# Optimization experiments

Hardware: AMD Instinct MI355X
Metric: run time of the kernel (lower is better)

The kernel has to match this reference:

```python
import jax, jax.numpy as jnp
import numpy as np

N_NODES, N_EDGES = 50000, 800000
IN_DIM, OUT_DIM, EDGE_DIM = 128, 128, 32
NUM_HEADS = 8
HEAD_DIM = OUT_DIM // NUM_HEADS
SCALE = HEAD_DIM ** -0.5


def setup_inputs() -> dict:
    key = jax.random.key(0)
    ks = jax.random.split(key, 8)
    def lin_w(k, fan_in, fan_out):
        # kaiming-uniform-ish init like nn.Linear
        bound = 1.0 / np.sqrt(fan_in)
        return jax.random.uniform(k, (fan_in, fan_out), jnp.float32, -bound, bound)
    return {
        "node_features": jax.random.normal(ks[0], (N_NODES, IN_DIM), jnp.float32),
        "edge_features": jax.random.normal(ks[1], (N_EDGES, EDGE_DIM), jnp.float32),
        "Wq": lin_w(ks[2], IN_DIM, OUT_DIM), "bq": jnp.zeros((OUT_DIM,), jnp.float32),
        "Wk": lin_w(ks[3], IN_DIM, OUT_DIM), "bk": jnp.zeros((OUT_DIM,), jnp.float32),
        "Wv": lin_w(ks[4], IN_DIM, OUT_DIM), "bv": jnp.zeros((OUT_DIM,), jnp.float32),
        "We": lin_w(ks[5], EDGE_DIM, OUT_DIM), "be": jnp.zeros((OUT_DIM,), jnp.float32),
        "edge_list": jax.random.randint(ks[6], (N_EDGES, 2), 0, N_NODES, jnp.int32),
        "num_nodes": N_NODES,
    }


def reference(node_features, edge_features, Wq, bq, Wk, bk, Wv, bv, We, be, edge_list, num_nodes):
    # node projections -> [N, H, D]
    Q = (node_features @ Wq + bq).reshape(-1, NUM_HEADS, HEAD_DIM)
    K = (node_features @ Wk + bk).reshape(-1, NUM_HEADS, HEAD_DIM)
    V = (node_features @ Wv + bv).reshape(-1, NUM_HEADS, HEAD_DIM)
    edge_bias = (edge_features @ We + be).reshape(-1, NUM_HEADS, HEAD_DIM)

    src = edge_list[:, 0]  # node_in
    dst = edge_list[:, 1]  # node_out

    # per-edge per-head scores: [E, H]
    scores = jnp.einsum("ehd,ehd->eh", Q[src], K[dst]) * SCALE + edge_bias.sum(-1)
    # NOTE: softmax over the HEADS axis (dim=1), exactly as in the source
    weights = jax.nn.softmax(scores, axis=1)

    # weighted messages gathered from src, scattered to dst: [E, H, D] -> [N, H, D]
    msg = V[src] * weights[..., None]
    node_updates = jax.ops.segment_sum(msg, dst, num_segments=num_nodes)
    return node_updates.reshape(num_nodes, OUT_DIM)
```

## Files before the change

kernel.cpp:

```cpp
#include <hip/hip_runtime.h>
#include <math.h>

#define IN_DIM   128
#define OUT_DIM  128
#define EDGE_DIM 32
#define NUM_HEADS 8
#define HEAD_DIM 16
#define SCALE 0.25f
#define CSTRIDE 16
#define MAXDEG 48

typedef __attribute__((ext_vector_type(8))) short bf16x8;
typedef __attribute__((ext_vector_type(4))) float f32x4;
typedef __attribute__((ext_vector_type(2))) float f32x2;
typedef __attribute__((ext_vector_type(4))) unsigned int u32x4;

__device__ inline unsigned short f2bf(float x) {
    unsigned int u = __float_as_uint(x);
    unsigned int r = u + 0x7fff + ((u >> 16) & 1);
    return (unsigned short)(r >> 16);
}
__device__ inline float bflo(unsigned int u) { return __uint_as_float(u << 16); }
__device__ inline float bfhi(unsigned int u) { return __uint_as_float(u & 0xffff0000u); }
__device__ inline f32x2 up2(unsigned int u) {
    f32x2 r; r[0] = bflo(u); r[1] = bfhi(u); return r;
}

__global__ __launch_bounds__(256) void setup_kernel(
    int* __restrict__ counts, int n_nodes, int nbz,
    const float* __restrict__ Wq, const float* __restrict__ Wk,
    const float* __restrict__ Wv, unsigned short* __restrict__ WtB, int nbw,
    const float* __restrict__ We, const float* __restrict__ be,
    float* __restrict__ WeR, float* __restrict__ beR,
    const float* __restrict__ X, unsigned short* __restrict__ Xb)
{
    const int bx = blockIdx.x;
    const int t  = threadIdx.x;
    if (bx < nbz) {
        const int i = bx * 256 + t;
        if (i < n_nodes) counts[i << 4] = 0;
    } else if (bx < nbz + nbw) {
        const int idx = (bx - nbz) * 256 + t;
        const int mat = idx >> 14;
        const int rem = idx & 16383;
        const int n = rem >> 7, k = rem & 127;
        const float* W = (mat == 0) ? Wq : (mat == 1) ? Wk : Wv;
        WtB[mat * 16384 + n * 128 + k] = f2bf(W[k * 128 + n]);
    } else if (bx == nbz + nbw) {
        const int k = t >> 3, h = t & 7;
        float s = 0.f;
#pragma unroll
        for (int d = 0; d < HEAD_DIM; ++d) s += We[k * OUT_DIM + h * HEAD_DIM + d];
        WeR[k * NUM_HEADS + h] = s;
        if (t < NUM_HEADS) {
            float sb = 0.f;
#pragma unroll
            for (int d = 0; d < HEAD_DIM; ++d) sb += be[t * HEAD_DIM + d];
            beR[t] = sb;
        }
    } else {
        const int i = (bx - (nbz + nbw + 1)) * 256 + t;
        if (i < n_nodes * 16) {
            const f32x4* xr = (const f32x4*)(X + (size_t)i * 8);
            const f32x4 x0 = xr[0], x1 = xr[1];
            u32x4 p;
            p[0] = (unsigned)f2bf(x0[0]) | ((unsigned)f2bf(x0[1]) << 16);
            p[1] = (unsigned)f2bf(x0[2]) | ((unsigned)f2bf(x0[3]) << 16);
            p[2] = (unsigned)f2bf(x1[0]) | ((unsigned)f2bf(x1[1]) << 16);
            p[3] = (unsigned)f2bf(x1[2]) | ((unsigned)f2bf(x1[3]) << 16);
            *(u32x4*)(Xb + (size_t)i * 8) = p;
        }
    }
}

__global__ __launch_bounds__(256) void qkv_kernel(
    const unsigned short* __restrict__ Xb, const unsigned short* __restrict__ WtB,
    const float* __restrict__ bq, const float* __restrict__ bk,
    const float* __restrict__ bv,
    unsigned short* __restrict__ QVb, unsigned short* __restrict__ Kb,
    int n_nodes, int nbm)
{
    __shared__ unsigned short shW[16384];
    const int bx = blockIdx.x;
    const int t  = threadIdx.x;

    const int which = bx / nbm;
    const int mb    = bx - which * nbm;
    const unsigned short* Wg = WtB + which * 16384;

#pragma unroll
    for (int kk = 0; kk < 8; ++kk) {
        const int c = kk * 256 + t;
        const u32x4 v = ((const u32x4*)Wg)[c];
        const int row = c >> 4;
        const int bir = (c & 15) << 4;
        *(u32x4*)((char*)shW + row * 256 + (bir ^ ((row & 7) << 4))) = v;
    }
    __syncthreads();

    const int wave = t >> 6, lane = t & 63;
    const int quad = lane >> 4, li = lane & 15;
    const int mbase = mb * 256 + wave * 64;

    int mrow[4];
#pragma unroll
    for (int m = 0; m < 4; ++m) {
        const int r_ = mbase + m * 16 + li;
        mrow[m] = (r_ < n_nodes) ? r_ : (n_nodes - 1);
    }

    f32x4 acc[4][8];
#pragma unroll
    for (int m = 0; m < 4; ++m)
#pragma unroll
        for (int nt = 0; nt < 8; ++nt) acc[m][nt] = (f32x4){0.f, 0.f, 0.f, 0.f};

#pragma unroll
    for (int ks = 0; ks < 4; ++ks) {
        bf16x8 a[4];
#pragma unroll
        for (int m = 0; m < 4; ++m)
            a[m] = *(const bf16x8*)(Xb + (size_t)mrow[m] * 128 + ks * 32 + quad * 8);
#pragma unroll
        for (int nt = 0; nt < 8; ++nt) {
            const int row = nt * 16 + li;
            const bf16x8 b = *(const bf16x8*)((const char*)shW + row * 256 +
                                ((ks * 64 + quad * 16) ^ ((row & 7) << 4)));
#pragma unroll
            for (int m = 0; m < 4; ++m)
                acc[m][nt] = __builtin_amdgcn_mfma_f32_16x16x32_bf16(a[m], b, acc[m][nt], 0, 0, 0);
        }
    }

    const float* bias = (which == 0) ? bq : (which == 1) ? bk : bv;
    float bv8[8];
#pragma unroll
    for (int nt = 0; nt < 8; ++nt) bv8[nt] = bias[nt * 16 + li];

    __syncthreads();

    unsigned short* stg = shW + wave * 2176;
    const int R = lane >> 2, cc4 = lane & 3;
#pragma unroll
    for (int m = 0; m < 4; ++m) {
#pragma unroll
        for (int nt = 0; nt < 8; ++nt)
#pragma unroll
            for (int r = 0; r < 4; ++r)
                stg[(quad * 4 + r) * 136 + nt * 16 + li] = f2bf(acc[m][nt][r] + bv8[nt]);
        __syncthreads();

        const int node = mbase + m * 16 + R;
        if (node < n_nodes) {
            const u32x4* s = (const u32x4*)(stg + R * 136 + cc4 * 32);
            u32x4 d0 = s[0], d1 = s[1], d2 = s[2], d3 = s[3];
            unsigned short* dp =
                (which == 0) ? (QVb + (size_t)node * 256 + cc4 * 32)
              : (which == 1) ? (Kb  + (size_t)node * 128 + cc4 * 32)
              :                (QVb + (size_t)node * 256 + 128 + cc4 * 32);
            u32x4* d = (u32x4*)dp;
            d[0] = d0; d[1] = d1; d[2] = d2; d[3] = d3;
        }
        __syncthreads();
    }
}

__global__ __launch_bounds__(256) void edge_kernel(
    const int* __restrict__ el, int* __restrict__ counts,
    const float* __restrict__ ef, const float* __restrict__ WeR,
    const float* __restrict__ beR, unsigned int* __restrict__ recs,
    int n_edges)
{
    const int e = blockIdx.x * 256 + threadIdx.x;
    if (e >= n_edges) return;
    const int2 ed = ((const int2*)el)[e];
    const int r = atomicAdd(&counts[ed.y << 4], 1);

    float acc[NUM_HEADS];
#pragma unroll
    for (int h = 0; h < NUM_HEADS; ++h) acc[h] = beR[h];

    const f32x4* efr = (const f32x4*)(ef + (size_t)e * EDGE_DIM);
#pragma unroll
    for (int kk = 0; kk < 8; ++kk) {
        const f32x4 f = efr[kk];
#pragma unroll
        for (int c = 0; c < 4; ++c) {
            const float* wr = WeR + (kk * 4 + c) * NUM_HEADS;
#pragma unroll
            for (int h = 0; h < NUM_HEADS; ++h)
                acc[h] = fmaf(f[c], wr[h], acc[h]);
        }
    }

    if (r < MAXDEG) {
        u32x4 r0, r1;
        r0[0] = (unsigned)ed.x;
        r0[1] = 0;
        r0[2] = (unsigned)f2bf(acc[0]) | ((unsigned)f2bf(acc[1]) << 16);
        r0[3] = (unsigned)f2bf(acc[2]) | ((unsigned)f2bf(acc[3]) << 16);
        r1[0] = (unsigned)f2bf(acc[4]) | ((unsigned)f2bf(acc[5]) << 16);
        r1[1] = (unsigned)f2bf(acc[6]) | ((unsigned)f2bf(acc[7]) << 16);
        r1[2] = 0; r1[3] = 0;
        u32x4* rp = (u32x4*)(recs + (size_t)(ed.y * MAXDEG + r) * 8);
        rp[0] = r0;
        rp[1] = r1;
    }
}

__global__ __launch_bounds__(256) void aggregate_kernel(
    const unsigned short* __restrict__ QVb, const unsigned short* __restrict__ Kb,
    const int* __restrict__ counts, const unsigned int* __restrict__ recs,
    float* __restrict__ out, int n_nodes, int nwtot)
{
    const int lane = threadIdx.x & 63;
    const int g = lane >> 3;
    const int h = lane & 7;
    const int ebd = 2 + (h >> 1);

    int node = (blockIdx.x * 256 + threadIdx.x) >> 6;
    if (node >= n_nodes) return;
    int cnt = counts[node << 4];
    if (cnt > MAXDEG) cnt = MAXDEG;

    for (;;) {
        const int nnode = node + nwtot;
        int ncnt = 0;
        if (nnode < n_nodes) {
            ncnt = counts[nnode << 4];
            if (ncnt > MAXDEG) ncnt = MAXDEG;
        }

        const int beg = node * MAXDEG;

        f32x2 kf[8];
        {
            const u32x4* kp = (const u32x4*)(Kb + (size_t)node * 128 + h * 16);
            const u32x4 ka = kp[0], kb_ = kp[1];
#pragma unroll
            for (int j = 0; j < 4; ++j) { kf[j] = up2(ka[j]); kf[4 + j] = up2(kb_[j]); }
        }

        f32x2 acc[8];
#pragma unroll
        for (int j = 0; j < 8; ++j) acc[j] = (f32x2){0.f, 0.f};

        if (cnt > 0) {
            const int last = cnt - 1;
            int s0 = g; if (s0 > last) s0 = last;
            const unsigned src_c = recs[(size_t)(beg + s0) * 8];
            unsigned ebw_c = recs[(size_t)(beg + s0) * 8 + ebd];
            const unsigned short* bp0 = QVb + (size_t)src_c * 256 + h * 16;
            u32x4 qa = *(const u32x4*)bp0;
            u32x4 qb = *(const u32x4*)(bp0 + 8);
            u32x4 va = *(const u32x4*)(bp0 + 128);
            u32x4 vb = *(const u32x4*)(bp0 + 136);
            int s1 = 8 + g; if (s1 > last) s1 = last;
            unsigned src_n = recs[(size_t)(beg + s1) * 8];
            unsigned ebw_n = recs[(size_t)(beg + s1) * 8 + ebd];

            for (int i = 0; i < cnt; i += 8) {
                int s2 = i + 16 + g; if (s2 > last) s2 = last;
                const unsigned src_f = recs[(size_t)(beg + s2) * 8];
                const unsigned ebw_f = recs[(size_t)(beg + s2) * 8 + ebd];
                const unsigned short* bp = QVb + (size_t)src_n * 256 + h * 16;
                const u32x4 qan = *(const u32x4*)bp;
                const u32x4 qbn = *(const u32x4*)(bp + 8);
                const u32x4 van = *(const u32x4*)(bp + 128);
                const u32x4 vbn = *(const u32x4*)(bp + 136);

                const float eb = (h & 1) ? bfhi(ebw_c) : bflo(ebw_c);
                f32x2 p2 = (f32x2){0.f, 0.f};
#pragma unroll
                for (int j = 0; j < 4; ++j) {
                    p2 += up2(qa[j]) * kf[j];
                    p2 += up2(qb[j]) * kf[4 + j];
                }
                const float score = fmaf(p2[0] + p2[1], SCALE, eb);

                const float ex = __expf(score);
                float den = ex;
                den += __shfl_xor(den, 1);
                den += __shfl_xor(den, 2);
                den += __shfl_xor(den, 4);
                float wgt = __fdividef(ex, den);
                if (i + g >= cnt) wgt = 0.f;
                const f32x2 w2 = (f32x2){wgt, wgt};
#pragma unroll
                for (int j = 0; j < 4; ++j) {
                    acc[j]     += up2(va[j]) * w2;
                    acc[4 + j] += up2(vb[j]) * w2;
                }

                qa = qan; qb = qbn; va = van; vb = vbn;
                ebw_c = ebw_n;
                src_n = src_f; ebw_n = ebw_f;
            }
        }

#pragma unroll
        for (int mask = 8; mask <= 32; mask <<= 1)
#pragma unroll
            for (int j = 0; j < 8; ++j) {
                f32x2 o;
                o[0] = __shfl_xor(acc[j][0], mask);
                o[1] = __shfl_xor(acc[j][1], mask);
                acc[j] += o;
            }

        float ox = 0.f, oy = 0.f;
#pragma unroll
        for (int j = 0; j < 8; ++j)
            if (g == j) { ox = acc[j][0]; oy = acc[j][1]; }
        *(float2*)(out + (size_t)node * OUT_DIM + h * 16 + g * 2) = make_float2(ox, oy);

        if (nnode >= n_nodes) break;
        node = nnode; cnt = ncnt;
    }
}

extern "C" void kernel_launch(void* const* d_in, const int* in_sizes, int n_in,
                              void* d_out, int out_size, void* d_ws, size_t ws_size,
                              hipStream_t stream)
{
    const float* X   = (const float*)d_in[0];
    const float* ef  = (const float*)d_in[1];
    const float* Wq  = (const float*)d_in[2];
    const float* bq  = (const float*)d_in[3];
    const float* Wk  = (const float*)d_in[4];
    const float* bk  = (const float*)d_in[5];
    const float* Wv  = (const float*)d_in[6];
    const float* bv  = (const float*)d_in[7];
    const float* We  = (const float*)d_in[8];
    const float* be  = (const float*)d_in[9];
    const int*   el  = (const int*)d_in[10];

    const int n_nodes = in_sizes[0] / IN_DIM;
    const int n_edges = in_sizes[10] / 2;

    char* w = (char*)d_ws;
    auto alloc = [&](size_t bytes) { char* p = w; w += (bytes + 255) & ~(size_t)255; return p; };

    unsigned short* QVb  = (unsigned short*)alloc((size_t)n_nodes * 256 * 2);
    unsigned short* Kb   = (unsigned short*)alloc((size_t)n_nodes * 128 * 2);
    unsigned short* WtB  = (unsigned short*)alloc((size_t)3 * 128 * 128 * 2);
    unsigned int*   recs = (unsigned int*)alloc((size_t)n_nodes * MAXDEG * 32);
    float* WeR   = (float*)alloc(EDGE_DIM * NUM_HEADS * 4);
    float* beR   = (float*)alloc(NUM_HEADS * 4);
    int* counts  = (int*)alloc((size_t)n_nodes * CSTRIDE * 4);

    unsigned short* Xb = (unsigned short*)recs;

    const int nbz = (n_nodes + 255) / 256;
    const int nbw = (3 * 128 * 128) / 256;
    const int nbx = (n_nodes * 16 + 255) / 256;
    setup_kernel<<<nbz + nbw + 1 + nbx, 256, 0, stream>>>(
        counts, n_nodes, nbz, Wq, Wk, Wv, WtB, nbw, We, be, WeR, beR, X, Xb);

    const int nbm = (n_nodes + 255) / 256;
    qkv_kernel<<<3 * nbm, 256, 0, stream>>>(
        Xb, WtB, bq, bk, bv, QVb, Kb, n_nodes, nbm);

    const int nbh = (n_edges + 255) / 256;
    edge_kernel<<<nbh, 256, 0, stream>>>(
        el, counts, ef, WeR, beR, recs, n_edges);

    int nblk = (n_nodes + 3) / 4;
    if (nblk > 2048) nblk = 2048;
    aggregate_kernel<<<nblk, 256, 0, stream>>>(
        QVb, Kb, counts, recs, (float*)d_out, n_nodes, nblk * 4);
}
```

Before: 331.4 us.

## Fuse QKV projection and edge-record kernels into one launch with separate Xb buffer

Merges the QKV GEMM kernel and the edge-scoring kernel into a single launch, with block ranges split between node GEMM work and per-edge work, so the two independent phases can overlap on the GPU. Xb gets its own buffer because it previously aliased recs, which the edge blocks now write concurrently. The GEMM part is restructured so each block does 64 nodes and all three weight matrices, reading B straight from global memory instead of staging weights in LDS. This reuses the A fragments but gives up LDS weight reuse and adds a bigger workspace footprint.

```diff
diff --git a/kernel.cpp b/kernel.cpp
--- a/kernel.cpp
+++ b/kernel.cpp
@@ -73,86 +73,104 @@
     }
 }
 
-__global__ __launch_bounds__(256) void qkv_kernel(
+__global__ __launch_bounds__(256) void mega_kernel(
     const unsigned short* __restrict__ Xb, const unsigned short* __restrict__ WtB,
     const float* __restrict__ bq, const float* __restrict__ bk,
     const float* __restrict__ bv,
     unsigned short* __restrict__ QVb, unsigned short* __restrict__ Kb,
-    int n_nodes, int nbm)
+    int n_nodes, int nbq,
+    const int* __restrict__ el, int* __restrict__ counts,
+    const float* __restrict__ ef, const float* __restrict__ WeR,
+    const float* __restrict__ beR, unsigned int* __restrict__ recs,
+    int n_edges)
 {
-    __shared__ unsigned short shW[16384];
+    __shared__ unsigned short stg[4][16][136];
     const int bx = blockIdx.x;
     const int t  = threadIdx.x;
 
-    const int which = bx / nbm;
-    const int mb    = bx - which * nbm;
-    const unsigned short* Wg = WtB + which * 16384;
-
-#pragma unroll
-    for (int kk = 0; kk < 8; ++kk) {
-        const int c = kk * 256 + t;
-        const u32x4 v = ((const u32x4*)Wg)[c];
-        const int row = c >> 4;
-        const int bir = (c & 15) << 4;
-        *(u32x4*)((char*)shW + row * 256 + (bir ^ ((row & 7) << 4))) = v;
+    if (bx >= nbq) {
+        const int e = (bx - nbq) * 256 + t;
+        if (e >= n_edges) return;
+        const int2 ed = ((const int2*)el)[e];
+        const int r = atomicAdd(&counts[ed.y << 4], 1);
+
+        float acc[NUM_HEADS];
+#pragma unroll
+        for (int h = 0; h < NUM_HEADS; ++h) acc[h] = beR[h];
+
+        const f32x4* efr = (const f32x4*)(ef + (size_t)e * EDGE_DIM);
+#pragma unroll
+        for (int kk = 0; kk < 8; ++kk) {
+            const f32x4 f = efr[kk];
+#pragma unroll
+            for (int c = 0; c < 4; ++c) {
+                const float* wr = WeR + (kk * 4 + c) * NUM_HEADS;
+#pragma unroll
+                for (int h = 0; h < NUM_HEADS; ++h)
+                    acc[h] = fmaf(f[c], wr[h], acc[h]);
+            }
+        }
+
+        if (r < MAXDEG) {
+            u32x4 r0, r1;
+            r0[0] = (unsigned)ed.x;
+            r0[1] = 0;
+            r0[2] = (unsigned)f2bf(acc[0]) | ((unsigned)f2bf(acc[1]) << 16);
+            r0[3] = (unsigned)f2bf(acc[2]) | ((unsigned)f2bf(acc[3]) << 16);
+            r1[0] = (unsigned)f2bf(acc[4]) | ((unsigned)f2bf(acc[5]) << 16);
+            r1[1] = (unsigned)f2bf(acc[6]) | ((unsigned)f2bf(acc[7]) << 16);
+            r1[2] = 0; r1[3] = 0;
+            u32x4* rp = (u32x4*)(recs + (size_t)(ed.y * MAXDEG + r) * 8);
+            rp[0] = r0;
+            rp[1] = r1;
+        }
+        return;
     }
-    __syncthreads();
 
     const int wave = t >> 6, lane = t & 63;
     const int quad = lane >> 4, li = lane & 15;
-    const int mbase = mb * 256 + wave * 64;
-
-    int mrow[4];
-#pragma unroll
-    for (int m = 0; m < 4; ++m) {
-        const int r_ = mbase + m * 16 + li;
-        mrow[m] = (r_ < n_nodes) ? r_ : (n_nodes - 1);
-    }
-
-    f32x4 acc[4][8];
-#pragma unroll
-    for (int m = 0; m < 4; ++m)
-#pragma unroll
-        for (int nt = 0; nt < 8; ++nt) acc[m][nt] = (f32x4){0.f, 0.f, 0.f, 0.f};
-
-#pragma unroll
-    for (int ks = 0; ks < 4; ++ks) {
-        bf16x8 a[4];
-#pragma unroll
-        for (int m = 0; m < 4; ++m)
-            a[m] = *(const bf16x8*)(Xb + (size_t)mrow[m] * 128 + ks * 32 + quad * 8);
+    const int m0 = bx * 64 + wave * 16;
+    int mrow = m0 + li;
+    if (mrow >= n_nodes) mrow = n_nodes - 1;
+
+    bf16x8 a[4];
+#pragma unroll
+    for (int ks = 0; ks < 4; ++ks)
+        a[ks] = *(const bf16x8*)(Xb + (size_t)mrow * 128 + ks * 32 + quad * 8);
+
+    const int R = lane >> 2;
+    const int cc4 = lane & 3;
+    const int node = m0 + R;
+
+#pragma unroll
+    for (int which = 0; which < 3; ++which) {
+        const float* bias = (which == 0) ? bq : (which == 1) ? bk : bv;
+        const unsigned short* Wg = WtB + which * 16384;
+
+        f32x4 acc[8];
+#pragma unroll
+        for (int nt = 0; nt < 8; ++nt) acc[nt] = (f32x4){0.f, 0.f, 0.f, 0.f};
+
+#pragma unroll
+        for (int ks = 0; ks < 4; ++ks) {
+#pragma unroll
+            for (int nt = 0; nt < 8; ++nt) {
+                const bf16x8 b = *(const bf16x8*)(Wg + (nt * 16 + li) * 128 + ks * 32 + quad * 8);
+                acc[nt] = __builtin_amdgcn_mfma_f32_16x16x32_bf16(a[ks], b, acc[nt], 0, 0, 0);
+            }
+        }
+
 #pragma unroll
         for (int nt = 0; nt < 8; ++nt) {
-            const int row = nt * 16 + li;
-            const bf16x8 b = *(const bf16x8*)((const char*)shW + row * 256 +
-                                ((ks * 64 + quad * 16) ^ ((row & 7) << 4)));
-#pragma unroll
-            for (int m = 0; m < 4; ++m)
-                acc[m][nt] = __builtin_amdgcn_mfma_f32_16x16x32_bf16(a[m], b, acc[m][nt], 0, 0, 0);
-        }
-    }
-
-    const float* bias = (which == 0) ? bq : (which == 1) ? bk : bv;
-    float bv8[8];
-#pragma unroll
-    for (int nt = 0; nt < 8; ++nt) bv8[nt] = bias[nt * 16 + li];
-
-    __syncthreads();
-
-    unsigned short* stg = shW + wave * 2176;
-    const int R = lane >> 2, cc4 = lane & 3;
-#pragma unroll
-    for (int m = 0; m < 4; ++m) {
-#pragma unroll
-        for (int nt = 0; nt < 8; ++nt)
+            const float bb = bias[nt * 16 + li];
 #pragma unroll
             for (int r = 0; r < 4; ++r)
-                stg[(quad * 4 + r) * 136 + nt * 16 + li] = f2bf(acc[m][nt][r] + bv8[nt]);
+                stg[wave][quad * 4 + r][nt * 16 + li] = f2bf(acc[nt][r] + bb);
+        }
         __syncthreads();
 
-        const int node = mbase + m * 16 + R;
         if (node < n_nodes) {
-            const u32x4* s = (const u32x4*)(stg + R * 136 + cc4 * 32);
+            const u32x4* s = (const u32x4*)(&stg[wave][R][cc4 * 32]);
             u32x4 d0 = s[0], d1 = s[1], d2 = s[2], d3 = s[3];
             unsigned short* dp =
                 (which == 0) ? (QVb + (size_t)node * 256 + cc4 * 32)
@@ -162,49 +180,6 @@
             d[0] = d0; d[1] = d1; d[2] = d2; d[3] = d3;
         }
         __syncthreads();
-    }
-}
-
-__global__ __launch_bounds__(256) void edge_kernel(
-    const int* __restrict__ el, int* __restrict__ counts,
-    const float* __restrict__ ef, const float* __restrict__ WeR,
-    const float* __restrict__ beR, unsigned int* __restrict__ recs,
-    int n_edges)
-{
-    const int e = blockIdx.x * 256 + threadIdx.x;
-    if (e >= n_edges) return;
-    const int2 ed = ((const int2*)el)[e];
-    const int r = atomicAdd(&counts[ed.y << 4], 1);
-
-    float acc[NUM_HEADS];
-#pragma unroll
-    for (int h = 0; h < NUM_HEADS; ++h) acc[h] = beR[h];
-
-    const f32x4* efr = (const f32x4*)(ef + (size_t)e * EDGE_DIM);
-#pragma unroll
-    for (int kk = 0; kk < 8; ++kk) {
-        const f32x4 f = efr[kk];
-#pragma unroll
-        for (int c = 0; c < 4; ++c) {
-            const float* wr = WeR + (kk * 4 + c) * NUM_HEADS;
-#pragma unroll
-            for (int h = 0; h < NUM_HEADS; ++h)
-                acc[h] = fmaf(f[c], wr[h], acc[h]);
-        }
-    }
-
-    if (r < MAXDEG) {
-        u32x4 r0, r1;
-        r0[0] = (unsigned)ed.x;
-        r0[1] = 0;
-        r0[2] = (unsigned)f2bf(acc[0]) | ((unsigned)f2bf(acc[1]) << 16);
-        r0[3] = (unsigned)f2bf(acc[2]) | ((unsigned)f2bf(acc[3]) << 16);
-        r1[0] = (unsigned)f2bf(acc[4]) | ((unsigned)f2bf(acc[5]) << 16);
-        r1[1] = (unsigned)f2bf(acc[6]) | ((unsigned)f2bf(acc[7]) << 16);
-        r1[2] = 0; r1[3] = 0;
-        u32x4* rp = (u32x4*)(recs + (size_t)(ed.y * MAXDEG + r) * 8);
-        rp[0] = r0;
-        rp[1] = r1;
     }
 }
 
@@ -345,11 +320,10 @@
     unsigned short* Kb   = (unsigned short*)alloc((size_t)n_nodes * 128 * 2);
     unsigned short* WtB  = (unsigned short*)alloc((size_t)3 * 128 * 128 * 2);
     unsigned int*   recs = (unsigned int*)alloc((size_t)n_nodes * MAXDEG * 32);
+    unsigned short* Xb   = (unsigned short*)alloc((size_t)n_nodes * 128 * 2);
     float* WeR   = (float*)alloc(EDGE_DIM * NUM_HEADS * 4);
     float* beR   = (float*)alloc(NUM_HEADS * 4);
     int* counts  = (int*)alloc((size_t)n_nodes * CSTRIDE * 4);
-
-    unsigned short* Xb = (unsigned short*)recs;
 
     const int nbz = (n_nodes + 255) / 256;
     const int nbw = (3 * 128 * 128) / 256;
@@ -357,12 +331,10 @@
     setup_kernel<<<nbz + nbw + 1 + nbx, 256, 0, stream>>>(
         counts, n_nodes, nbz, Wq, Wk, Wv, WtB, nbw, We, be, WeR, beR, X, Xb);
 
-    const int nbm = (n_nodes + 255) / 256;
-    qkv_kernel<<<3 * nbm, 256, 0, stream>>>(
-        Xb, WtB, bq, bk, bv, QVb, Kb, n_nodes, nbm);
-
+    const int nbq = (n_nodes + 63) / 64;
     const int nbh = (n_edges + 255) / 256;
-    edge_kernel<<<nbh, 256, 0, stream>>>(
+    mega_kernel<<<nbq + nbh, 256, 0, stream>>>(
+        Xb, WtB, bq, bk, bv, QVb, Kb, n_nodes, nbq,
         el, counts, ef, WeR, beR, recs, n_edges);
 
     int nblk = (n_nodes + 3) / 4;
```

Measured after the change: 332.6 us. About the same (+0.3%).
